# Performance work log

Hardware: AMD Instinct MI355X
Metric: run time of the kernel (lower is better)

## Reference

```python
import jax, jax.numpy as jnp
import numpy as np

TAU = 2.0
V_TH = 1.0
ALPHA = 2.0  # ATan surrogate alpha (spikingjelly default)

@jax.custom_vjp
def atan_heaviside(x):
    # Forward: Heaviside spike; backward: ATan surrogate gradient.
    return (x >= 0).astype(x.dtype)

def _atan_fwd(x):
    return atan_heaviside(x), x

def _atan_bwd(x, g):
    sg = (ALPHA / 2.0) / (1.0 + (jnp.pi / 2.0 * ALPHA * x) ** 2)
    return (g * sg,)

atan_heaviside.defvjp(_atan_fwd, _atan_bwd)

def lif_scan(cur):
    # cur: [T, B, F] input currents. LIF: H = V + (X - V)/tau; S = H >= v_th; hard reset V = H*(1-S).
    def step(v, x_t):
        h = v + (x_t - v) / TAU
        s = atan_heaviside(h - V_TH)
        v_new = h * (1.0 - s)
        return v_new, s
    v0 = jnp.zeros(cur.shape[1:], dtype=cur.dtype)
    _, spikes = jax.lax.scan(step, v0, cur)
    return spikes

def setup_inputs() -> dict:
    key = jax.random.key(0)
    k1, k2 = jax.random.split(key)
    T, B, F_in, F_out = 64, 256, 1024, 1024
    x = jax.random.normal(k1, (T, B, F_in), dtype=jnp.float32)
    W = jax.random.normal(k2, (F_out, F_in), dtype=jnp.float32) * (1.0 / np.sqrt(F_in))
    return {"x": x, "W": W}

def reference(x, W):
    # Linear projection over all timesteps, then multi-step LIF recurrence.
    cur = jnp.einsum('tbf,of->tbo', x, W)  # [T, B, F_out]
    return lif_scan(cur)
```

## Files before the change

kernel.cpp:

```cpp
#include <hip/hip_runtime.h>


#define T_DIM 64
#define B_DIM 256
#define F_DIM 1024
#define K_DIM 1024
#define M_DIM 16384
#define COLS  (B_DIM * F_DIM)
#define KP    2048
#define MARGIN 6e-5f
#define LIST_CAP 32768

typedef __attribute__((ext_vector_type(8))) short short8;
typedef __attribute__((ext_vector_type(4))) float floatx4;

#define ASYNC_CP16(gp, lp)                                                     \
    __builtin_amdgcn_global_load_lds(                                          \
        (const __attribute__((address_space(1))) unsigned int*)(gp),           \
        (__attribute__((address_space(3))) unsigned int*)(lp), 16, 0, 0)

__device__ inline unsigned short f32_to_bf16_rne(float f) {
    unsigned int u = __builtin_bit_cast(unsigned int, f);
    unsigned int r = (u + 0x7FFFu + ((u >> 16) & 1u)) >> 16;
    return (unsigned short)r;
}
__device__ inline float bf16_to_f32(unsigned short h) {
    unsigned int u = ((unsigned int)h) << 16;
    return __builtin_bit_cast(float, u);
}

__global__ __launch_bounds__(256) void split_kernel(
    const float* __restrict__ x, const float* __restrict__ Wm,
    unsigned short* __restrict__ A, unsigned short* __restrict__ B,
    unsigned int* __restrict__ counter)
{
    if (blockIdx.x == 0 && threadIdx.x == 0) *counter = 0;
    const int blk = blockIdx.x;
    const float* in;
    unsigned short* dst;
    int g;
    int orow;
    if (blk < 16384) {
        g = blk * 256 + threadIdx.x;
        int e = g * 4;
        int row = e >> 10;
        orow = ((row & 255) << 6) | (row >> 8);
        in = x; dst = A;
    } else {
        g = (blk - 16384) * 256 + threadIdx.x;
        int e = g * 4;
        orow = e >> 10;
        in = Wm; dst = B;
    }
    int k = (g * 4) & 1023;
    float4 v = reinterpret_cast<const float4*>(in)[g];
    ushort4 h, l;
    float f;
    f = v.x; h.x = f32_to_bf16_rne(f); l.x = f32_to_bf16_rne(f - bf16_to_f32(h.x));
    f = v.y; h.y = f32_to_bf16_rne(f); l.y = f32_to_bf16_rne(f - bf16_to_f32(h.y));
    f = v.z; h.z = f32_to_bf16_rne(f); l.z = f32_to_bf16_rne(f - bf16_to_f32(h.z));
    f = v.w; h.w = f32_to_bf16_rne(f); l.w = f32_to_bf16_rne(f - bf16_to_f32(h.w));
    reinterpret_cast<ushort4*>(dst)[(size_t)orow * (KP / 4) + (k >> 2)] = h;
    reinterpret_cast<ushort4*>(dst)[(size_t)orow * (KP / 4) + 256 + (k >> 2)] = l;
}

__global__ __launch_bounds__(512, 2) void gemm_scan_kernel(
    const unsigned short* __restrict__ A,
    const unsigned short* __restrict__ B,
    float* __restrict__ out,
    unsigned int* __restrict__ counter, unsigned int* __restrict__ list)
{
    __shared__ unsigned short Ah0[128 * 32], Al0[128 * 32];
    __shared__ unsigned short Bh0[256 * 32], Bl0[256 * 32];
    __shared__ unsigned short Ah1[128 * 32], Al1[128 * 32];
    __shared__ unsigned short Bh1[256 * 32], Bl1[256 * 32];

    const int tid  = threadIdx.x;
    const int lane = tid & 63;
    const int wv   = tid >> 6;
    const int lid = blockIdx.x;
    const int mt  = ((lid & 7) << 4) | (lid >> 5);
    const int nt  = (lid >> 3) & 3;
    const int m0  = mt * 128;
    const int n0  = nt * 256;
    const int wm  = (wv & 1) * 64;
    const int wn  = (wv >> 1) * 64;

    floatx4 acc[4][4] = {};

    const int srow = tid >> 2;
    const int slin = (tid & 3) * 8;
    const int ssw  = (((tid & 3) ^ ((srow >> 1) & 3)) * 8);
    const int lrow = lane & 15;
    const int q    = lane >> 4;
    const int rsw  = (lrow >> 1) & 3;
    const int sl   = (q ^ rsw) * 8;

    const unsigned short* Ab = A + (size_t)m0 * KP;
    const unsigned short* Bb = B + (size_t)n0 * KP;

    const unsigned short* ga_h  = Ab + (size_t)srow * KP + ssw;
    const unsigned short* ga_l  = ga_h + 1024;
    const unsigned short* gb0_h = Bb + (size_t)srow * KP + ssw;
    const unsigned short* gb0_l = gb0_h + 1024;
    const unsigned short* gb1_h = gb0_h + (size_t)128 * KP;
    const unsigned short* gb1_l = gb1_h + 1024;

    const int ldsA  = srow * 32 + slin;
    const int ldsB1 = (srow + 128) * 32 + slin;

    int aoff[4], boff[4];
#pragma unroll
    for (int i = 0; i < 4; ++i) aoff[i] = (wm + i * 16 + lrow) * 32 + sl;
#pragma unroll
    for (int j = 0; j < 4; ++j) boff[j] = (wn + j * 16 + lrow) * 32 + sl;

#define STAGE(AhB, AlB, BhB, BlB, kk) do {                                     \
        ASYNC_CP16(ga_h + (kk),  &AhB[ldsA]);                                  \
        ASYNC_CP16(ga_l + (kk),  &AlB[ldsA]);                                  \
        ASYNC_CP16(gb0_h + (kk), &BhB[ldsA]);                                  \
        ASYNC_CP16(gb1_h + (kk), &BhB[ldsB1]);                                 \
        ASYNC_CP16(gb0_l + (kk), &BlB[ldsA]);                                  \
        ASYNC_CP16(gb1_l + (kk), &BlB[ldsB1]);                                 \
    } while (0)

#define COMPUTE(AhB, AlB, BhB, BlB) do {                                       \
        short8 ah[4], al[4], bh[4], bl[4];                                     \
        _Pragma("unroll")                                                      \
        for (int i = 0; i < 4; ++i) {                                          \
            ah[i] = *reinterpret_cast<const short8*>(&AhB[aoff[i]]);           \
            al[i] = *reinterpret_cast<const short8*>(&AlB[aoff[i]]);           \
        }                                                                      \
        _Pragma("unroll")                                                      \
        for (int j = 0; j < 4; ++j) {                                          \
            bh[j] = *reinterpret_cast<const short8*>(&BhB[boff[j]]);           \
            bl[j] = *reinterpret_cast<const short8*>(&BlB[boff[j]]);           \
        }                                                                      \
        __builtin_amdgcn_s_setprio(1);                                         \
        _Pragma("unroll")                                                      \
        for (int i = 0; i < 4; ++i)                                            \
            _Pragma("unroll")                                                  \
            for (int j = 0; j < 4; ++j)                                        \
                acc[i][j] = __builtin_amdgcn_mfma_f32_16x16x32_bf16(           \
                    ah[i], bh[j], acc[i][j], 0, 0, 0);                         \
        _Pragma("unroll")                                                      \
        for (int i = 0; i < 4; ++i)                                            \
            _Pragma("unroll")                                                  \
            for (int j = 0; j < 4; ++j)                                        \
                acc[i][j] = __builtin_amdgcn_mfma_f32_16x16x32_bf16(           \
                    al[i], bh[j], acc[i][j], 0, 0, 0);                         \
        _Pragma("unroll")                                                      \
        for (int i = 0; i < 4; ++i)                                            \
            _Pragma("unroll")                                                  \
            for (int j = 0; j < 4; ++j)                                        \
                acc[i][j] = __builtin_amdgcn_mfma_f32_16x16x32_bf16(           \
                    ah[i], bl[j], acc[i][j], 0, 0, 0);                         \
        __builtin_amdgcn_s_setprio(0);                                         \
    } while (0)

    STAGE(Ah0, Al0, Bh0, Bl0, 0);
    __syncthreads();

#pragma unroll 1
    for (int kt = 0; kt < 32; kt += 2) {
        STAGE(Ah1, Al1, Bh1, Bl1, (kt + 1) * 32);
        COMPUTE(Ah0, Al0, Bh0, Bl0);
        __syncthreads();
        if (kt + 2 < 32) STAGE(Ah0, Al0, Bh0, Bl0, (kt + 2) * 32);
        COMPUTE(Ah1, Al1, Bh1, Bl1);
        __syncthreads();
    }

#undef STAGE
#undef COMPUTE

    const int col = lane & 15;
    const int b_g = mt * 2 + (wv & 1);

    unsigned int fmask = 0;
#pragma unroll
    for (int j = 0; j < 4; ++j) {
        float v = 0.f;
        bool fl = false;
#pragma unroll
        for (int i = 0; i < 4; ++i) {
#pragma unroll
            for (int qq = 0; qq < 4; ++qq) {
                if (q == qq) {
#pragma unroll
                    for (int r = 0; r < 4; ++r) {
                        float cu = acc[i][j][r];
                        float h = v + (cu - v) * 0.5f;
                        float d = h - 1.0f;
                        bool sp = (d >= 0.f);
                        fl |= (fabsf(d) < MARGIN);
                        acc[i][j][r] = sp ? 1.0f : 0.0f;
                        v = sp ? 0.f : h;
                    }
                }
                v = __shfl(v, qq * 16 + col, 64);
            }
        }
        if (fl) fmask |= (1u << j);
    }
    fmask |= __shfl_xor(fmask, 16, 64);
    fmask |= __shfl_xor(fmask, 32, 64);

    float* outp = out + (size_t)b_g * F_DIM;
#pragma unroll
    for (int i = 0; i < 4; ++i)
#pragma unroll
        for (int j = 0; j < 4; ++j)
#pragma unroll
            for (int r = 0; r < 4; ++r) {
                int t = i * 16 + q * 4 + r;
                int o = n0 + wn + j * 16 + col;
                outp[(size_t)t * COLS + o] = acc[i][j][r];
            }

    if (q == 0 && fmask) {
        for (int j = 0; j < 4; ++j)
            if (fmask & (1u << j)) {
                unsigned int idx = atomicAdd(counter, 1u);
                if (idx < LIST_CAP)
                    list[idx] = (unsigned int)((b_g << 10) | (n0 + wn + j * 16 + col));
            }
    }
}

__global__ __launch_bounds__(256) void fixup_kernel(
    const float* __restrict__ x, const float* __restrict__ W,
    const unsigned int* __restrict__ counter, const unsigned int* __restrict__ list,
    float* __restrict__ out)
{
    __shared__ double curd[T_DIM];
    __shared__ float wrow[K_DIM];
    unsigned int n = *counter;
    if (n > LIST_CAP) n = LIST_CAP;
    const int wv = threadIdx.x >> 6, lane = threadIdx.x & 63;

    for (unsigned int idx = blockIdx.x; idx < n; idx += gridDim.x) {
        const unsigned int c = list[idx];
        const int b = c >> 10, o = c & 1023;
        __syncthreads();
        for (int k = threadIdx.x; k < K_DIM; k += 256) wrow[k] = W[(size_t)o * K_DIM + k];
        __syncthreads();
        for (int it = 0; it < 16; ++it) {
            const int t = it * 4 + wv;
            const float* xp = x + (size_t)t * COLS + (size_t)b * F_DIM + lane * 16;
            double s = 0.0;
#pragma unroll
            for (int qq = 0; qq < 4; ++qq) {
                float4 xv = reinterpret_cast<const float4*>(xp)[qq];
                float4 wq = *reinterpret_cast<const float4*>(&wrow[lane * 16 + qq * 4]);
                s += (double)xv.x * (double)wq.x + (double)xv.y * (double)wq.y +
                     (double)xv.z * (double)wq.z + (double)xv.w * (double)wq.w;
            }
#pragma unroll
            for (int off = 32; off > 0; off >>= 1) s += __shfl_down(s, off, 64);
            if (lane == 0) curd[t] = s;
        }
        __syncthreads();
        if (threadIdx.x == 0) {
            double v = 0.0;
            for (int t = 0; t < T_DIM; ++t) {
                double h = v + (curd[t] - v) * 0.5;
                bool s = (h >= 1.0);
                out[(size_t)t * COLS + c] = s ? 1.0f : 0.0f;
                v = s ? 0.0 : h;
            }
        }
        __syncthreads();
    }
}

#define TILE 64
#define KC 32
#define XS_LD 36
#define SC_LD 65

__global__ __launch_bounds__(256) void lif_fused_kernel(
    const float* __restrict__ x, const float* __restrict__ Wm, float* __restrict__ out)
{
    __shared__ __align__(16) unsigned char smem_raw[TILE * SC_LD * sizeof(double)];
    float* sf = reinterpret_cast<float*>(smem_raw);
    double* sd = reinterpret_cast<double*>(smem_raw);
    float* Xs = sf;
    float* Ws = sf + TILE * XS_LD;

    const int b = blockIdx.y;
    const int o0 = blockIdx.x * TILE;
    const int tid = threadIdx.x;
    const int tx = tid & 15, ty = tid >> 4;

    double acc[4][4];
#pragma unroll
    for (int i = 0; i < 4; ++i)
#pragma unroll
        for (int j = 0; j < 4; ++j) acc[i][j] = 0.0;

    const int r = tid >> 3, c4 = (tid & 7) * 4;
    const float* xbase = x + (size_t)b * F_DIM;

    for (int k0 = 0; k0 < K_DIM; k0 += KC) {
        __syncthreads();
        float4 xv0 = *reinterpret_cast<const float4*>(xbase + (size_t)r * COLS + k0 + c4);
        float4 xv1 = *reinterpret_cast<const float4*>(xbase + (size_t)(r + 32) * COLS + k0 + c4);
        *reinterpret_cast<float4*>(Xs + r * XS_LD + c4) = xv0;
        *reinterpret_cast<float4*>(Xs + (r + 32) * XS_LD + c4) = xv1;
        float4 wv0 = *reinterpret_cast<const float4*>(Wm + (size_t)(o0 + r) * K_DIM + k0 + c4);
        float4 wv1 = *reinterpret_cast<const float4*>(Wm + (size_t)(o0 + r + 32) * K_DIM + k0 + c4);
        *reinterpret_cast<float4*>(Ws + r * XS_LD + c4) = wv0;
        *reinterpret_cast<float4*>(Ws + (r + 32) * XS_LD + c4) = wv1;
        __syncthreads();
#pragma unroll 4
        for (int kk = 0; kk < KC; ++kk) {
            double xa[4], wb[4];
#pragma unroll
            for (int i = 0; i < 4; ++i) xa[i] = (double)Xs[(4 * ty + i) * XS_LD + kk];
#pragma unroll
            for (int j = 0; j < 4; ++j) wb[j] = (double)Ws[(4 * tx + j) * XS_LD + kk];
#pragma unroll
            for (int i = 0; i < 4; ++i)
#pragma unroll
                for (int j = 0; j < 4; ++j) acc[i][j] = fma(xa[i], wb[j], acc[i][j]);
        }
    }
    __syncthreads();
#pragma unroll
    for (int i = 0; i < 4; ++i)
#pragma unroll
        for (int j = 0; j < 4; ++j) sd[(4 * ty + i) * SC_LD + (4 * tx + j)] = acc[i][j];
    __syncthreads();
    if (tid < TILE) {
        double v = 0.0;
        float* outp = out + (size_t)b * F_DIM + o0 + tid;
        for (int t = 0; t < T_DIM; ++t) {
            double cu = sd[t * SC_LD + tid];
            double h = v + (cu - v) * 0.5;
            bool s = (h >= 1.0);
            outp[(size_t)t * COLS] = s ? 1.0f : 0.0f;
            v = s ? 0.0 : h;
        }
    }
}

extern "C" void kernel_launch(void* const* d_in, const int* in_sizes, int n_in,
                              void* d_out, int out_size, void* d_ws, size_t ws_size,
                              hipStream_t stream) {
    const float* x = (const float*)d_in[0];
    const float* Wm = (const float*)d_in[1];
    float* out = (float*)d_out;

    const size_t OFF_A   = 0;
    const size_t OFF_B   = OFF_A + (size_t)M_DIM * KP * 2;
    const size_t OFF_CNT = OFF_B + (size_t)F_DIM * KP * 2;
    const size_t OFF_LST = OFF_CNT + 256;
    const size_t NEEDED  = OFF_LST + (size_t)LIST_CAP * 4;

    if (ws_size < NEEDED) {
        dim3 grid(F_DIM / TILE, B_DIM, 1);
        lif_fused_kernel<<<grid, dim3(256), 0, stream>>>(x, Wm, out);
        return;
    }

    unsigned char* ws = (unsigned char*)d_ws;
    unsigned short* Abuf = (unsigned short*)(ws + OFF_A);
    unsigned short* Bbuf = (unsigned short*)(ws + OFF_B);
    unsigned int* counter = (unsigned int*)(ws + OFF_CNT);
    unsigned int* list = (unsigned int*)(ws + OFF_LST);

    split_kernel<<<dim3(16384 + 1024), dim3(256), 0, stream>>>(x, Wm, Abuf, Bbuf, counter);
    gemm_scan_kernel<<<dim3(512), dim3(512), 0, stream>>>(Abuf, Bbuf, out, counter, list);
    fixup_kernel<<<dim3(512), dim3(256), 0, stream>>>(x, Wm, counter, list, out);
}
```

Baseline: 228.8 us.

## Double GEMM M-tile to 256 rows and add hard waitcnt barriers

```diff
diff --git a/kernel.cpp b/kernel.cpp
--- a/kernel.cpp
+++ b/kernel.cpp
@@ -18,6 +18,13 @@
     __builtin_amdgcn_global_load_lds(                                          \
         (const __attribute__((address_space(1))) unsigned int*)(gp),           \
         (__attribute__((address_space(3))) unsigned int*)(lp), 16, 0, 0)
+
+#define HARD_SYNC() do {                                                       \
+        __builtin_amdgcn_sched_barrier(0);                                     \
+        asm volatile("s_waitcnt vmcnt(0) lgkmcnt(0)" ::: "memory");            \
+        __syncthreads();                                                       \
+        __builtin_amdgcn_sched_barrier(0);                                     \
+    } while (0)
 
 __device__ inline unsigned short f32_to_bf16_rne(float f) {
     unsigned int u = __builtin_bit_cast(unsigned int, f);
@@ -70,23 +77,23 @@
     float* __restrict__ out,
     unsigned int* __restrict__ counter, unsigned int* __restrict__ list)
 {
-    __shared__ unsigned short Ah0[128 * 32], Al0[128 * 32];
+    __shared__ unsigned short Ah0[256 * 32], Al0[256 * 32];
     __shared__ unsigned short Bh0[256 * 32], Bl0[256 * 32];
-    __shared__ unsigned short Ah1[128 * 32], Al1[128 * 32];
+    __shared__ unsigned short Ah1[256 * 32], Al1[256 * 32];
     __shared__ unsigned short Bh1[256 * 32], Bl1[256 * 32];
 
     const int tid  = threadIdx.x;
     const int lane = tid & 63;
     const int wv   = tid >> 6;
     const int lid = blockIdx.x;
-    const int mt  = ((lid & 7) << 4) | (lid >> 5);
+    const int mt  = ((lid & 7) << 3) | (lid >> 5);
     const int nt  = (lid >> 3) & 3;
-    const int m0  = mt * 128;
+    const int m0  = mt * 256;
     const int n0  = nt * 256;
-    const int wm  = (wv & 1) * 64;
+    const int wm  = (wv & 1) * 128;
     const int wn  = (wv >> 1) * 64;
 
-    floatx4 acc[4][4] = {};
+    floatx4 acc[8][4] = {};
 
     const int srow = tid >> 2;
     const int slin = (tid & 3) * 8;
@@ -96,135 +103,142 @@
     const int rsw  = (lrow >> 1) & 3;
     const int sl   = (q ^ rsw) * 8;
 
-    const unsigned short* Ab = A + (size_t)m0 * KP;
-    const unsigned short* Bb = B + (size_t)n0 * KP;
-
-    const unsigned short* ga_h  = Ab + (size_t)srow * KP + ssw;
-    const unsigned short* ga_l  = ga_h + 1024;
-    const unsigned short* gb0_h = Bb + (size_t)srow * KP + ssw;
-    const unsigned short* gb0_l = gb0_h + 1024;
-    const unsigned short* gb1_h = gb0_h + (size_t)128 * KP;
-    const unsigned short* gb1_l = gb1_h + 1024;
+    const size_t RKP = (size_t)128 * KP;
+    const unsigned short* ga_h = A + (size_t)(m0 + srow) * KP + ssw;
+    const unsigned short* ga_l = ga_h + 1024;
+    const unsigned short* gb_h = B + (size_t)(n0 + srow) * KP + ssw;
+    const unsigned short* gb_l = gb_h + 1024;
 
     const int ldsA  = srow * 32 + slin;
-    const int ldsB1 = (srow + 128) * 32 + slin;
-
-    int aoff[4], boff[4];
-#pragma unroll
-    for (int i = 0; i < 4; ++i) aoff[i] = (wm + i * 16 + lrow) * 32 + sl;
+    const int ldsA2 = (srow + 128) * 32 + slin;
+
+    int aoff[8], boff[4];
+#pragma unroll
+    for (int i = 0; i < 8; ++i) aoff[i] = (wm + i * 16 + lrow) * 32 + sl;
 #pragma unroll
     for (int j = 0; j < 4; ++j) boff[j] = (wn + j * 16 + lrow) * 32 + sl;
 
 #define STAGE(AhB, AlB, BhB, BlB, kk) do {                                     \
-        ASYNC_CP16(ga_h + (kk),  &AhB[ldsA]);                                  \
-        ASYNC_CP16(ga_l + (kk),  &AlB[ldsA]);                                  \
-        ASYNC_CP16(gb0_h + (kk), &BhB[ldsA]);                                  \
-        ASYNC_CP16(gb1_h + (kk), &BhB[ldsB1]);                                 \
-        ASYNC_CP16(gb0_l + (kk), &BlB[ldsA]);                                  \
-        ASYNC_CP16(gb1_l + (kk), &BlB[ldsB1]);                                 \
+        ASYNC_CP16(ga_h + (kk),       &AhB[ldsA]);                             \
+        ASYNC_CP16(ga_h + RKP + (kk), &AhB[ldsA2]);                            \
+        ASYNC_CP16(ga_l + (kk),       &AlB[ldsA]);                             \
+        ASYNC_CP16(ga_l + RKP + (kk), &AlB[ldsA2]);                            \
+        ASYNC_CP16(gb_h + (kk),       &BhB[ldsA]);                             \
+        ASYNC_CP16(gb_h + RKP + (kk), &BhB[ldsA2]);                            \
+        ASYNC_CP16(gb_l + (kk),       &BlB[ldsA]);                             \
+        ASYNC_CP16(gb_l + RKP + (kk), &BlB[ldsA2]);                            \
     } while (0)
 
 #define COMPUTE(AhB, AlB, BhB, BlB) do {                                       \
-        short8 ah[4], al[4], bh[4], bl[4];                                     \
+        short8 ah[8], al[8];                                                   \
         _Pragma("unroll")                                                      \
-        for (int i = 0; i < 4; ++i) {                                          \
+        for (int i = 0; i < 8; ++i) {                                          \
             ah[i] = *reinterpret_cast<const short8*>(&AhB[aoff[i]]);           \
             al[i] = *reinterpret_cast<const short8*>(&AlB[aoff[i]]);           \
         }                                                                      \
         _Pragma("unroll")                                                      \
-        for (int j = 0; j < 4; ++j) {                                          \
-            bh[j] = *reinterpret_cast<const short8*>(&BhB[boff[j]]);           \
-            bl[j] = *reinterpret_cast<const short8*>(&BlB[boff[j]]);           \
+        for (int jh = 0; jh < 2; ++jh) {                                       \
+            short8 bh[2], bl[2];                                               \
+            _Pragma("unroll")                                                  \
+            for (int j2 = 0; j2 < 2; ++j2) {                                   \
+                bh[j2] = *reinterpret_cast<const short8*>(&BhB[boff[jh * 2 + j2]]); \
+                bl[j2] = *reinterpret_cast<const short8*>(&BlB[boff[jh * 2 + j2]]); \
+            }                                                                  \
+            __builtin_amdgcn_s_setprio(1);                                     \
+            _Pragma("unroll")                                                  \
+            for (int i = 0; i < 8; ++i)                                        \
+                _Pragma("unroll")                                              \
+                for (int j2 = 0; j2 < 2; ++j2)                                 \
+                    acc[i][jh * 2 + j2] = __builtin_amdgcn_mfma_f32_16x16x32_bf16( \
+                        ah[i], bh[j2], acc[i][jh * 2 + j2], 0, 0, 0);          \
+            _Pragma("unroll")                                                  \
+            for (int i = 0; i < 8; ++i)                                        \
+                _Pragma("unroll")                                              \
+                for (int j2 = 0; j2 < 2; ++j2)                                 \
+                    acc[i][jh * 2 + j2] = __builtin_amdgcn_mfma_f32_16x16x32_bf16( \
+                        al[i], bh[j2], acc[i][jh * 2 + j2], 0, 0, 0);          \
+            _Pragma("unroll")                                                  \
+            for (int i = 0; i < 8; ++i)                                        \
+                _Pragma("unroll")                                              \
+                for (int j2 = 0; j2 < 2; ++j2)                                 \
+                    acc[i][jh * 2 + j2] = __builtin_amdgcn_mfma_f32_16x16x32_bf16( \
+                        ah[i], bl[j2], acc[i][jh * 2 + j2], 0, 0, 0);          \
+            __builtin_amdgcn_s_setprio(0);                                     \
         }                                                                      \
-        __builtin_amdgcn_s_setprio(1);                                         \
-        _Pragma("unroll")                                                      \
-        for (int i = 0; i < 4; ++i)                                            \
-            _Pragma("unroll")                                                  \
-            for (int j = 0; j < 4; ++j)                                        \
-                acc[i][j] = __builtin_amdgcn_mfma_f32_16x16x32_bf16(           \
-                    ah[i], bh[j], acc[i][j], 0, 0, 0);                         \
-        _Pragma("unroll")                                                      \
-        for (int i = 0; i < 4; ++i)                                            \
-            _Pragma("unroll")                                                  \
-            for (int j = 0; j < 4; ++j)                                        \
-                acc[i][j] = __builtin_amdgcn_mfma_f32_16x16x32_bf16(           \
-                    al[i], bh[j], acc[i][j], 0, 0, 0);                         \
-        _Pragma("unroll")                                                      \
-        for (int i = 0; i < 4; ++i)                                            \
-            _Pragma("unroll")                                                  \
-            for (int j = 0; j < 4; ++j)                                        \
-                acc[i][j] = __builtin_amdgcn_mfma_f32_16x16x32_bf16(           \
-                    ah[i], bl[j], acc[i][j], 0, 0, 0);                         \
-        __builtin_amdgcn_s_setprio(0);                                         \
     } while (0)
 
     STAGE(Ah0, Al0, Bh0, Bl0, 0);
-    __syncthreads();
+    HARD_SYNC();
 
 #pragma unroll 1
     for (int kt = 0; kt < 32; kt += 2) {
         STAGE(Ah1, Al1, Bh1, Bl1, (kt + 1) * 32);
         COMPUTE(Ah0, Al0, Bh0, Bl0);
-        __syncthreads();
+        HARD_SYNC();
         if (kt + 2 < 32) STAGE(Ah0, Al0, Bh0, Bl0, (kt + 2) * 32);
         COMPUTE(Ah1, Al1, Bh1, Bl1);
-        __syncthreads();
+        HARD_SYNC();
     }
 
 #undef STAGE
 #undef COMPUTE
 
     const int col = lane & 15;
-    const int b_g = mt * 2 + (wv & 1);
+    const int b_base = mt * 4 + (wv & 1) * 2;
 
     unsigned int fmask = 0;
 #pragma unroll
-    for (int j = 0; j < 4; ++j) {
-        float v = 0.f;
-        bool fl = false;
-#pragma unroll
-        for (int i = 0; i < 4; ++i) {
-#pragma unroll
-            for (int qq = 0; qq < 4; ++qq) {
-                if (q == qq) {
-#pragma unroll
-                    for (int r = 0; r < 4; ++r) {
-                        float cu = acc[i][j][r];
-                        float h = v + (cu - v) * 0.5f;
-                        float d = h - 1.0f;
-                        bool sp = (d >= 0.f);
-                        fl |= (fabsf(d) < MARGIN);
-                        acc[i][j][r] = sp ? 1.0f : 0.0f;
-                        v = sp ? 0.f : h;
+    for (int hb = 0; hb < 2; ++hb) {
+#pragma unroll
+        for (int j = 0; j < 4; ++j) {
+            float v = 0.f;
+            bool fl = false;
+#pragma unroll
+            for (int i4 = 0; i4 < 4; ++i4) {
+                const int i = hb * 4 + i4;
+#pragma unroll
+                for (int qq = 0; qq < 4; ++qq) {
+                    if (q == qq) {
+#pragma unroll
+                        for (int r = 0; r < 4; ++r) {
+                            float cu = acc[i][j][r];
+                            float hm = v + (cu - v) * 0.5f;
+                            float d = hm - 1.0f;
+                            bool sp = (d >= 0.f);
+                            fl |= (fabsf(d) < MARGIN);
+                            acc[i][j][r] = sp ? 1.0f : 0.0f;
+                            v = sp ? 0.f : hm;
+                        }
                     }
+                    v = __shfl(v, qq * 16 + col, 64);
                 }
-                v = __shfl(v, qq * 16 + col, 64);
             }
-        }
-        if (fl) fmask |= (1u << j);
+            if (fl) fmask |= (1u << (hb * 4 + j));
+        }
     }
     fmask |= __shfl_xor(fmask, 16, 64);
     fmask |= __shfl_xor(fmask, 32, 64);
 
-    float* outp = out + (size_t)b_g * F_DIM;
-#pragma unroll
-    for (int i = 0; i < 4; ++i)
+#pragma unroll
+    for (int i = 0; i < 8; ++i) {
+        float* outp = out + (size_t)(b_base + (i >> 2)) * F_DIM;
+        const int tb = (i & 3) * 16 + q * 4;
 #pragma unroll
         for (int j = 0; j < 4; ++j)
 #pragma unroll
-            for (int r = 0; r < 4; ++r) {
-                int t = i * 16 + q * 4 + r;
-                int o = n0 + wn + j * 16 + col;
-                outp[(size_t)t * COLS + o] = acc[i][j][r];
-            }
+            for (int r = 0; r < 4; ++r)
+                outp[(size_t)(tb + r) * COLS + (n0 + wn + j * 16 + col)] = acc[i][j][r];
+    }
 
     if (q == 0 && fmask) {
-        for (int j = 0; j < 4; ++j)
-            if (fmask & (1u << j)) {
-                unsigned int idx = atomicAdd(counter, 1u);
-                if (idx < LIST_CAP)
-                    list[idx] = (unsigned int)((b_g << 10) | (n0 + wn + j * 16 + col));
-            }
+        for (int hb = 0; hb < 2; ++hb)
+            for (int j = 0; j < 4; ++j)
+                if (fmask & (1u << (hb * 4 + j))) {
+                    unsigned int idx = atomicAdd(counter, 1u);
+                    if (idx < LIST_CAP)
+                        list[idx] = (unsigned int)(((b_base + hb) << 10) |
+                                                   (n0 + wn + j * 16 + col));
+                }
     }
 }
 
@@ -371,6 +385,6 @@
     unsigned int* list = (unsigned int*)(ws + OFF_LST);
 
     split_kernel<<<dim3(16384 + 1024), dim3(256), 0, stream>>>(x, Wm, Abuf, Bbuf, counter);
-    gemm_scan_kernel<<<dim3(512), dim3(512), 0, stream>>>(Abuf, Bbuf, out, counter, list);
+    gemm_scan_kernel<<<dim3(256), dim3(512), 0, stream>>>(Abuf, Bbuf, out, counter, list);
     fixup_kernel<<<dim3(512), dim3(256), 0, stream>>>(x, Wm, counter, list, out);
 }
```

Result: faster. 222.5 us (-2.7%).
